# Kernel tuning notes

Measured on AMD Instinct MI355X. Metric: run time of the kernel, lower is better.

The kernel has to match this reference:

```python
import jax, jax.numpy as jnp
import numpy as np
import math

B, S, D, H = 4, 512, 1024, 16
DH = D // H
DQ = D // 4
MIN_STEPS, MAX_STEPS = 4, 12
THR = 1e-4


def lin(t, w, b):
    # torch Linear convention: w is (out, in)
    return jnp.einsum('...i,oi->...o', t, w) + b


def gelu(t):
    return jax.nn.gelu(t, approximate=False)  # torch nn.GELU() exact


def layernorm(t, g, b):
    m = t.mean(-1, keepdims=True)
    v = jnp.mean(jnp.square(t - m), axis=-1, keepdims=True)
    return (t - m) * jax.lax.rsqrt(v + 1e-5) * g + b


def _forward(h, x, ig_w1, ig_b1, ig_w2, ig_b2, wq, bq, wk, bk, wv, bv, wo, bo,
             g1_w1, g1_b1, g1_w2, g1_b2, gate_logits, ln_g, ln_b,
             sp_w1, sp_b1, sp_w2, sp_b2):
    # adaptive step count: steps = base + floor(sigmoid(MLP(mean_pool(h))).mean() * extra)
    pooled = h.mean(axis=1)  # (B, D)
    extra = jax.nn.sigmoid(lin(gelu(lin(pooled, sp_w1, sp_b1)), sp_w2, sp_b2)).mean()
    num_steps = jnp.minimum(
        MIN_STEPS + jnp.floor(extra * (MAX_STEPS - MIN_STEPS)).astype(jnp.int32), MAX_STEPS)

    gw = jax.nn.softmax(gate_logits)  # gate weights over the 3 gates
    scale = 1.0 / math.sqrt(DH)

    def step(carry, i):
        h, active = carry
        # G1 gate (G2/G3 multiply zero memory/expert outputs -> drop)
        G1 = jax.nn.sigmoid(lin(gelu(lin(h, g1_w1, g1_b1)), g1_w2, g1_b2)) * gw[0]
        # Phi: input-gated blend + raw multi-head self-attention
        gate = jax.nn.sigmoid(
            lin(gelu(lin(jnp.concatenate([h, x], axis=-1), ig_w1, ig_b1)), ig_w2, ig_b2))
        blended = gate * h + (1.0 - gate) * x
        q = lin(blended, wq, bq).reshape(B, S, H, DH)
        k = lin(blended, wk, bk).reshape(B, S, H, DH)
        v = lin(blended, wv, bv).reshape(B, S, H, DH)
        attn = jax.nn.softmax(jnp.einsum('bqhd,bkhd->bhqk', q, k) * scale, axis=-1)
        ctx = jnp.einsum('bhqk,bkhd->bqhd', attn, v).reshape(B, S, D)
        phi = lin(ctx, wo, bo)
        h_new = layernorm(h + G1 * phi, ln_g, ln_b)
        res = jnp.linalg.norm(h_new - h) / (jnp.linalg.norm(h) + 1e-8)
        act_i = active & (i < num_steps)
        h = jnp.where(act_i, h_new, h)
        active = act_i & jnp.logical_not((i >= MIN_STEPS) & (res < THR))
        return (h, active), None

    (h, _), _ = jax.lax.scan(step, (h, jnp.array(True)), jnp.arange(MAX_STEPS))
    return h


def setup_inputs() -> dict:
    key = jax.random.key(0)
    ks = jax.random.split(key, 16)
    f32 = jnp.float32

    def W(k, out_d, in_d):
        return jax.random.normal(k, (out_d, in_d), f32) * (1.0 / np.sqrt(in_d))

    return {
        'h': jax.random.normal(ks[0], (B, S, D), f32),
        'x': jax.random.normal(ks[1], (B, S, D), f32),
        # PhiLayer input_gate: Linear(2D, D/4) -> GELU -> Linear(D/4, D) -> Sigmoid
        'ig_w1': W(ks[2], DQ, 2 * D), 'ig_b1': jnp.zeros((DQ,), f32),
        'ig_w2': W(ks[3], D, DQ), 'ig_b2': jnp.zeros((D,), f32),
        # QKV / out projections (xavier-ish, zero bias)
        'wq': W(ks[4], D, D), 'bq': jnp.zeros((D,), f32),
        'wk': W(ks[5], D, D), 'bk': jnp.zeros((D,), f32),
        'wv': W(ks[6], D, D), 'bv': jnp.zeros((D,), f32),
        'wo': W(ks[7], D, D), 'bo': jnp.zeros((D,), f32),
        # Gating gate #1 MLP (only G1 contributes; memory/experts are zero)
        'g1_w1': W(ks[8], DQ, D), 'g1_b1': jnp.zeros((DQ,), f32),
        'g1_w2': W(ks[9], D, DQ), 'g1_b2': jnp.zeros((D,), f32),
        'gate_logits': jnp.ones((3,), f32),  # nn.Parameter(torch.ones(3))
        # LayerNorm
        'ln_g': jnp.ones((D,), f32), 'ln_b': jnp.zeros((D,), f32),
        # step predictor: Linear(D, D/4) -> GELU -> Linear(D/4, 1)
        'sp_w1': W(ks[10], DQ, D), 'sp_b1': jnp.zeros((DQ,), f32),
        'sp_w2': W(ks[11], 1, DQ), 'sp_b2': jnp.zeros((1,), f32),
    }


def reference(h, x, ig_w1, ig_b1, ig_w2, ig_b2, wq, bq, wk, bk, wv, bv, wo, bo,
              g1_w1, g1_b1, g1_w2, g1_b2, gate_logits, ln_g, ln_b,
              sp_w1, sp_b1, sp_w2, sp_b2):
    return _forward(h, x, ig_w1, ig_b1, ig_w2, ig_b2, wq, bq, wk, bk, wv, bv, wo, bo,
                    g1_w1, g1_b1, g1_w2, g1_b2, gate_logits, ln_g, ln_b,
                    sp_w1, sp_b1, sp_w2, sp_b2)
```

## Files before the change

kernel.cpp:

```cpp
#include <hip/hip_runtime.h>
#include <hip/hip_bf16.h>


#define B_   4
#define S_   512
#define D_   1024
#define H_   16
#define DH_  64
#define MSEQ 2048

typedef short short8 __attribute__((ext_vector_type(8)));
typedef float floatx4 __attribute__((ext_vector_type(4)));

static constexpr size_t OFF_H    = 0;
static constexpr size_t OFF_X    = 2097152;
static constexpr size_t OFF_HXB  = 4194304;
static constexpr size_t OFF_T2B  = 6291456;
static constexpr size_t OFF_T1B  = 6553600;
static constexpr size_t OFF_G1B  = 6815744;
static constexpr size_t OFF_QKVB = 7864320;
static constexpr size_t OFF_U    = 7864320;
static constexpr size_t OFF_CTXB = 11010048;
static constexpr size_t OFF_WARE = 12058624;
static constexpr size_t OFF_BIAS = 14811136;
static constexpr size_t OFF_POOL = 14817792;
static constexpr size_t OFF_SPT  = 14821888;
static constexpr size_t OFF_PPART= 14822912;
static constexpr size_t OFF_SCAL = 14888448;

static constexpr int W_WIG1 = 0;
static constexpr int W_WIG2 = 524288;
static constexpr int W_WG1  = 786432;
static constexpr int W_WG2  = 1048576;
static constexpr int W_QKV  = 1310720;
static constexpr int W_WO   = 4456448;
static constexpr int W_TOT  = 5505024;
static constexpr int B_TOT  = 6656;

__device__ __forceinline__ float bf2f(unsigned int u) {
  return __uint_as_float((u & 0xFFFFu) << 16);
}
__device__ __forceinline__ short f2bs(float f) {
  __hip_bfloat16 b = __float2bfloat16(f);
  return *reinterpret_cast<short*>(&b);
}
__device__ __forceinline__ unsigned int pk2(float lo, float hi) {
  return (unsigned int)(unsigned short)f2bs(lo) | ((unsigned int)(unsigned short)f2bs(hi) << 16);
}
__device__ __forceinline__ float ldf(const void* p, size_t i, int f32m) {
  return f32m ? ((const float*)p)[i] : bf2f(((const unsigned short*)p)[i]);
}
__device__ __forceinline__ float gelu_f(float x) {
  return 0.5f * x * (1.0f + erff(x * 0.70710678118654752440f));
}
__device__ __forceinline__ float sig_f(float x) {
  return 1.0f / (1.0f + expf(-x));
}
__device__ __forceinline__ void gl_lds16(const short* gp, short* lp) {
  __builtin_amdgcn_global_load_lds(
      (const __attribute__((address_space(1))) unsigned int*)gp,
      (__attribute__((address_space(3))) unsigned int*)lp, 16, 0, 0);
}
__device__ __forceinline__ float wave_sum(float v) {
  #pragma unroll
  for (int off = 32; off > 0; off >>= 1) v += __shfl_xor(v, off);
  return v;
}

__global__ void detect_kernel(const void* ln_g, int* dtf) {
  *dtf = (((const unsigned int*)ln_g)[0] == 0x3F800000u) ? 1 : 0;
}

struct RepackPtrs {
  const void* w[8];
  const void* b[8];
};

__global__ __launch_bounds__(256) void repack_all_kernel(
    const int* __restrict__ dtf, RepackPtrs ps,
    short* __restrict__ wdst, float* __restrict__ bdst) {
  const int f32m = *dtf;
  int i = blockIdx.x * 256 + threadIdx.x;
  if (i < W_TOT) {
    const int off[9] = {0, 524288, 786432, 1048576, 1310720, 2359296, 3407872, 4456448, W_TOT};
    int seg = 0;
    #pragma unroll
    for (int s = 1; s < 8; s++) seg += (i >= off[s]) ? 1 : 0;
    wdst[i] = f2bs(ldf(ps.w[seg], i - off[seg], f32m));
  } else if (i < W_TOT + B_TOT) {
    int j = i - W_TOT;
    const int off[9] = {0, 256, 1280, 1536, 2560, 3584, 4608, 5632, B_TOT};
    int seg = 0;
    #pragma unroll
    for (int s = 1; s < 8; s++) seg += (j >= off[s]) ? 1 : 0;
    bdst[j] = ldf(ps.b[seg], j - off[seg], f32m);
  }
}

__global__ __launch_bounds__(256) void cvt_in_kernel(
    const int* __restrict__ dtf, const void* __restrict__ hb,
    const void* __restrict__ xb, float* __restrict__ h, float* __restrict__ x,
    short* __restrict__ hxb, int n) {
  int f32m = *dtf;
  int i = blockIdx.x * 256 + threadIdx.x;
  if (i < n) {
    float hv = ldf(hb, i, f32m);
    float xv = ldf(xb, i, f32m);
    h[i] = hv;
    x[i] = xv;
    int row = i >> 10, col = i & 1023;
    hxb[(size_t)row * 2048 + col] = f2bs(hv);
    hxb[(size_t)row * 2048 + 1024 + col] = f2bs(xv);
  }
}

__global__ __launch_bounds__(256) void cvt_out_kernel(
    const int* __restrict__ dtf, const float* __restrict__ h, void* __restrict__ out, int n) {
  int f32m = *dtf;
  int i = blockIdx.x * 256 + threadIdx.x;
  if (i < n) {
    if (f32m) ((float*)out)[i] = h[i];
    else ((__hip_bfloat16*)out)[i] = __float2bfloat16(h[i]);
  }
}

__global__ __launch_bounds__(256) void pool_s1_kernel(
    const float* __restrict__ H, float* __restrict__ part) {
  int b = blockIdx.x, c = blockIdx.y, tid = threadIdx.x;
  const float* p = H + ((size_t)b * S_ + c * 32) * D_;
  #pragma unroll
  for (int rep = 0; rep < 4; rep++) {
    int d = rep * 256 + tid;
    float s = 0.f;
    for (int r = 0; r < 32; r++) s += p[(size_t)r * D_ + d];
    part[((size_t)b * 16 + c) * D_ + d] = s;
  }
}
__global__ __launch_bounds__(256) void pool_s2_kernel(
    const float* __restrict__ part, float* __restrict__ pooled) {
  int i = blockIdx.x * 256 + threadIdx.x;
  int b = i >> 10, d = i & 1023;
  float s = 0.f;
  #pragma unroll
  for (int c = 0; c < 16; c++) s += part[((size_t)b * 16 + c) * D_ + d];
  pooled[i] = s * (1.0f / (float)S_);
}

__device__ __forceinline__ float blk_sum256(float v, float* sm, int tid) {
  #pragma unroll
  for (int off = 32; off > 0; off >>= 1) v += __shfl_xor(v, off);
  __syncthreads();
  if ((tid & 63) == 0) sm[tid >> 6] = v;
  __syncthreads();
  return sm[0] + sm[1] + sm[2] + sm[3];
}

__global__ __launch_bounds__(256) void sp1_kernel(
    const int* __restrict__ dtf, const float* __restrict__ pooled,
    const void* __restrict__ w1, const void* __restrict__ b1,
    float* __restrict__ spt) {
  __shared__ float sm[4];
  const int f32m = *dtf;
  int j = blockIdx.x, tid = threadIdx.x;
  float s[4] = {0.f, 0.f, 0.f, 0.f};
  #pragma unroll
  for (int r = 0; r < 4; r++) {
    int k = tid * 4 + r;
    float w = ldf(w1, (size_t)j * D_ + k, f32m);
    s[0] += pooled[k] * w;
    s[1] += pooled[1024 + k] * w;
    s[2] += pooled[2048 + k] * w;
    s[3] += pooled[3072 + k] * w;
  }
  #pragma unroll
  for (int b = 0; b < 4; b++) {
    float t = blk_sum256(s[b], sm, tid);
    __syncthreads();
    if (tid == 0) spt[b * 256 + j] = gelu_f(t + ldf(b1, j, f32m));
  }
}

__global__ __launch_bounds__(256) void sp2_kernel(
    const int* __restrict__ dtf, const float* __restrict__ spt,
    const void* __restrict__ w2, const void* __restrict__ b2,
    const void* __restrict__ glog,
    int* __restrict__ num_steps, int* __restrict__ active,
    float* __restrict__ gw0, float* __restrict__ ssd, float* __restrict__ ssh) {
  __shared__ float z[4];
  const int f32m = *dtf;
  int tid = threadIdx.x;
  int wave = tid >> 6, lane = tid & 63;
  {
    int b = wave;
    float s = spt[b * 256 + lane]       * ldf(w2, lane, f32m) +
              spt[b * 256 + lane + 64]  * ldf(w2, lane + 64, f32m) +
              spt[b * 256 + lane + 128] * ldf(w2, lane + 128, f32m) +
              spt[b * 256 + lane + 192] * ldf(w2, lane + 192, f32m);
    #pragma unroll
    for (int off = 32; off > 0; off >>= 1) s += __shfl_xor(s, off);
    if (lane == 0) z[b] = sig_f(s + ldf(b2, 0, f32m));
  }
  __syncthreads();
  if (tid == 0) {
    float extra = 0.25f * (z[0] + z[1] + z[2] + z[3]);
    int ns = 4 + (int)floorf(extra * 8.0f);
    if (ns > 12) ns = 12;
    *num_steps = ns;
    *active = 1;
    *ssd = 0.f; *ssh = 0.f;
    float g0 = ldf(glog, 0, f32m);
    float g1 = ldf(glog, 1, f32m);
    float g2 = ldf(glog, 2, f32m);
    float mx = fmaxf(g0, fmaxf(g1, g2));
    float e0 = expf(g0 - mx), e1 = expf(g1 - mx), e2 = expf(g2 - mx);
    *gw0 = e0 / (e0 + e1 + e2);
  }
}

__global__ void control_kernel(int i, int* __restrict__ active, int* __restrict__ cur,
                               const int* __restrict__ num_steps,
                               float* __restrict__ ssd, float* __restrict__ ssh) {
  if (i > 0) {
    int prevf = *cur;
    if (prevf && (i - 1) >= 4) {
      float res = sqrtf(*ssd) / (sqrtf(*ssh) + 1e-8f);
      if (res < 1e-4f) *active = 0;
    }
  }
  *cur = ((*active) && (i < *num_steps)) ? 1 : 0;
  *ssd = 0.f; *ssh = 0.f;
}

enum { EPI_NONE = 0, EPI_GELU = 1, EPI_SIGSCALE = 2, EPI_BLEND = 3, EPI_RESADD = 4 };

template <int EPI, int BM, int BN>
__device__ __forceinline__ void mgemm_core(
    short* As, short* Bs,
    const short* __restrict__ A, int lda,
    const short* __restrict__ W, const float* __restrict__ bias, int K, int N,
    float* __restrict__ Cf, short* __restrict__ Cb,
    const float* __restrict__ aux1, const float* __restrict__ aux2f,
    const short* __restrict__ aux2b, const float* __restrict__ scale_ptr,
    int m0, int n0) {
  constexpr int FM = (BM / 2) / 16;
  constexpr int FN = (BN / 2) / 16;
  constexpr int CPA = (BM / 16) / 4;
  constexpr int CPB = (BN / 16) / 4;
  const int tid = threadIdx.x;
  const int lane = tid & 63, wv_ = tid >> 6;
  const int wm = (wv_ >> 1) * (BM / 2), wn = (wv_ & 1) * (BN / 2);
  const int srow = lane >> 2, scol = (lane & 3) * 8;
  const int frow = lane & 15, fk = (lane >> 4) * 8;

  floatx4 acc[FM][FN];
  #pragma unroll
  for (int i = 0; i < FM; i++)
    #pragma unroll
    for (int j = 0; j < FN; j++) acc[i][j] = (floatx4){0.f, 0.f, 0.f, 0.f};

  for (int k0 = 0; k0 < K; k0 += 32) {
    __syncthreads();
    #pragma unroll
    for (int c = 0; c < CPA; c++) {
      int q = wv_ * CPA + c;
      gl_lds16(A + (size_t)(m0 + q * 16 + srow) * lda + k0 + scol, As + q * 512);
    }
    #pragma unroll
    for (int c = 0; c < CPB; c++) {
      int q = wv_ * CPB + c;
      gl_lds16(W + (size_t)(n0 + q * 16 + srow) * K + k0 + scol, Bs + q * 512);
    }
    __syncthreads();
    short8 a[FM], b[FN];
    #pragma unroll
    for (int i = 0; i < FM; i++)
      a[i] = *reinterpret_cast<const short8*>(&As[(wm + i * 16 + frow) * 32 + fk]);
    #pragma unroll
    for (int j = 0; j < FN; j++)
      b[j] = *reinterpret_cast<const short8*>(&Bs[(wn + j * 16 + frow) * 32 + fk]);
    #pragma unroll
    for (int i = 0; i < FM; i++)
      #pragma unroll
      for (int j = 0; j < FN; j++)
        acc[i][j] = __builtin_amdgcn_mfma_f32_16x16x32_bf16(a[i], b[j], acc[i][j], 0, 0, 0);
  }

  float gwv = 0.f;
  if (EPI == EPI_SIGSCALE) gwv = *scale_ptr;
  const int rq = (lane >> 4) * 4;
  #pragma unroll
  for (int i = 0; i < FM; i++) {
    #pragma unroll
    for (int j = 0; j < FN; j++) {
      int n = n0 + wn + j * 16 + (lane & 15);
      float bv = bias[n];
      #pragma unroll
      for (int r = 0; r < 4; r++) {
        int m = m0 + wm + i * 16 + rq + r;
        size_t off = (size_t)m * N + n;
        float v = acc[i][j][r] + bv;
        if (EPI == EPI_GELU) {
          Cb[off] = f2bs(gelu_f(v));
        } else if (EPI == EPI_SIGSCALE) {
          Cb[off] = f2bs(sig_f(v) * gwv);
        } else if (EPI == EPI_BLEND) {
          float s = sig_f(v);
          Cb[off] = f2bs(s * aux1[off] + (1.f - s) * aux2f[off]);
        } else if (EPI == EPI_RESADD) {
          Cf[off] = aux1[off] + bf2f((unsigned short)aux2b[off]) * v;
        } else {
          Cb[off] = f2bs(v);
        }
      }
    }
  }
}

template <int EPI, int BM, int BN>
__global__ __launch_bounds__(256) void mgemm(
    const int* __restrict__ flag, const short* __restrict__ A, int lda,
    const short* __restrict__ W, const float* __restrict__ bias, int K, int N,
    float* __restrict__ Cf, short* __restrict__ Cb,
    const float* __restrict__ aux1, const float* __restrict__ aux2f,
    const short* __restrict__ aux2b, const float* __restrict__ scale_ptr) {
  if (*flag == 0) return;
  __shared__ short As[BM * 32];
  __shared__ short Bs[BN * 32];
  mgemm_core<EPI, BM, BN>(As, Bs, A, lda, W, bias, K, N, Cf, Cb,
                          aux1, aux2f, aux2b, scale_ptr,
                          blockIdx.y * BM, blockIdx.x * BN);
}

__global__ __launch_bounds__(256) void gate1_kernel(
    const int* __restrict__ flag, const short* __restrict__ hxb,
    const short* __restrict__ warena, const float* __restrict__ biasA,
    short* __restrict__ t2b, short* __restrict__ t1b) {
  if (*flag == 0) return;
  __shared__ short As[64 * 32];
  __shared__ short Bs[64 * 32];
  if (blockIdx.z == 0)
    mgemm_core<EPI_GELU, 64, 64>(As, Bs, hxb, 2048, warena + W_WIG1, biasA + 0,
                                 2048, 256, nullptr, t2b, nullptr, nullptr, nullptr,
                                 nullptr, blockIdx.y * 64, blockIdx.x * 64);
  else
    mgemm_core<EPI_GELU, 64, 64>(As, Bs, hxb, 2048, warena + W_WG1, biasA + 1280,
                                 1024, 256, nullptr, t1b, nullptr, nullptr, nullptr,
                                 nullptr, blockIdx.y * 64, blockIdx.x * 64);
}

__global__ __launch_bounds__(256) void gate2_kernel(
    const int* __restrict__ flag, const short* __restrict__ t2b,
    const short* __restrict__ t1b, const short* __restrict__ warena,
    const float* __restrict__ biasA, short* __restrict__ bldb,
    short* __restrict__ g1b, const float* __restrict__ h,
    const float* __restrict__ xf, const float* __restrict__ gw0) {
  if (*flag == 0) return;
  __shared__ short As[128 * 32];
  __shared__ short Bs[64 * 32];
  if (blockIdx.z == 0)
    mgemm_core<EPI_BLEND, 128, 64>(As, Bs, t2b, 256, warena + W_WIG2, biasA + 256,
                                   256, 1024, nullptr, bldb, h, xf, nullptr,
                                   nullptr, blockIdx.y * 128, blockIdx.x * 64);
  else
    mgemm_core<EPI_SIGSCALE, 128, 64>(As, Bs, t1b, 256, warena + W_WG2, biasA + 1536,
                                      256, 1024, nullptr, g1b, nullptr, nullptr,
                                      nullptr, gw0, blockIdx.y * 128, blockIdx.x * 64);
}

#define AP_ 72
__global__ __launch_bounds__(256) void attn_kernel(
    const int* __restrict__ flag, const short* __restrict__ qkv,
    short* __restrict__ ctxb) {
  if (*flag == 0) return;
  __shared__ short Ks[64 * AP_];
  __shared__ short Vt[64 * AP_];
  __shared__ short Ps[64 * AP_];
  const int tid = threadIdx.x;
  const int lane = tid & 63, wv = tid >> 6;
  const int ln15 = lane & 15, quad = lane >> 4;
  const int qt = blockIdx.x, hh = blockIdx.y, b = blockIdx.z;
  const int wm = wv * 16;
  const size_t rowbase = (size_t)b * S_;
  const int hcol = hh * DH_;
  const float scale = 0.125f;

  short8 qa[2];
  {
    const short* qp = qkv + (rowbase + qt * 64 + wm + ln15) * 3072 + hcol + quad * 8;
    qa[0] = *reinterpret_cast<const short8*>(qp);
    qa[1] = *reinterpret_cast<const short8*>(qp + 32);
  }
  const int skk = tid >> 2, scg = (tid & 3) * 16;

  float mrow[4] = {-1e30f, -1e30f, -1e30f, -1e30f};
  float lrow[4] = {0.f, 0.f, 0.f, 0.f};
  floatx4 accO[4];
  #pragma unroll
  for (int j = 0; j < 4; j++) accO[j] = (floatx4){0.f, 0.f, 0.f, 0.f};

  for (int kt = 0; kt < 8; kt++) {
    __syncthreads();
    {
      const short* gk = qkv + (rowbase + kt * 64 + skk) * 3072 + 1024 + hcol + scg;
      uint4 k0 = *reinterpret_cast<const uint4*>(gk);
      uint4 k1 = *reinterpret_cast<const uint4*>(gk + 8);
      *reinterpret_cast<uint4*>(&Ks[skk * AP_ + scg]) = k0;
      *reinterpret_cast<uint4*>(&Ks[skk * AP_ + scg + 8]) = k1;
      short8 v0 = *reinterpret_cast<const short8*>(gk + 1024);
      short8 v1 = *reinterpret_cast<const short8*>(gk + 1032);
      #pragma unroll
      for (int j = 0; j < 8; j++) Vt[(scg + j) * AP_ + skk] = v0[j];
      #pragma unroll
      for (int j = 0; j < 8; j++) Vt[(scg + 8 + j) * AP_ + skk] = v1[j];
    }
    __syncthreads();

    floatx4 sc[4];
    #pragma unroll
    for (int nf = 0; nf < 4; nf++) {
      short8 b0 = *reinterpret_cast<const short8*>(&Ks[(nf * 16 + ln15) * AP_ + quad * 8]);
      short8 b1 = *reinterpret_cast<const short8*>(&Ks[(nf * 16 + ln15) * AP_ + 32 + quad * 8]);
      floatx4 s = (floatx4){0.f, 0.f, 0.f, 0.f};
      s = __builtin_amdgcn_mfma_f32_16x16x32_bf16(qa[0], b0, s, 0, 0, 0);
      s = __builtin_amdgcn_mfma_f32_16x16x32_bf16(qa[1], b1, s, 0, 0, 0);
      sc[nf] = s;
    }

    float prob[4][4];
    #pragma unroll
    for (int r = 0; r < 4; r++) {
      float lm = fmaxf(fmaxf(sc[0][r], sc[1][r]), fmaxf(sc[2][r], sc[3][r])) * scale;
      lm = fmaxf(lm, __shfl_xor(lm, 1));
      lm = fmaxf(lm, __shfl_xor(lm, 2));
      lm = fmaxf(lm, __shfl_xor(lm, 4));
      lm = fmaxf(lm, __shfl_xor(lm, 8));
      float mn = fmaxf(mrow[r], lm);
      float alpha = expf(mrow[r] - mn);
      float ls = 0.f;
      #pragma unroll
      for (int nf = 0; nf < 4; nf++) {
        float p = expf(sc[nf][r] * scale - mn);
        prob[nf][r] = p;
        ls += p;
      }
      ls += __shfl_xor(ls, 1);
      ls += __shfl_xor(ls, 2);
      ls += __shfl_xor(ls, 4);
      ls += __shfl_xor(ls, 8);
      lrow[r] = lrow[r] * alpha + ls;
      mrow[r] = mn;
      #pragma unroll
      for (int df = 0; df < 4; df++) accO[df][r] *= alpha;
    }
    #pragma unroll
    for (int nf = 0; nf < 4; nf++)
      #pragma unroll
      for (int r = 0; r < 4; r++)
        Ps[(wm + quad * 4 + r) * AP_ + nf * 16 + ln15] = f2bs(prob[nf][r]);
    __syncthreads();

    short8 pa0 = *reinterpret_cast<const short8*>(&Ps[(wm + ln15) * AP_ + quad * 8]);
    short8 pa1 = *reinterpret_cast<const short8*>(&Ps[(wm + ln15) * AP_ + 32 + quad * 8]);
    #pragma unroll
    for (int df = 0; df < 4; df++) {
      short8 bv0 = *reinterpret_cast<const short8*>(&Vt[(df * 16 + ln15) * AP_ + quad * 8]);
      short8 bv1 = *reinterpret_cast<const short8*>(&Vt[(df * 16 + ln15) * AP_ + 32 + quad * 8]);
      accO[df] = __builtin_amdgcn_mfma_f32_16x16x32_bf16(pa0, bv0, accO[df], 0, 0, 0);
      accO[df] = __builtin_amdgcn_mfma_f32_16x16x32_bf16(pa1, bv1, accO[df], 0, 0, 0);
    }
  }

  float inv[4];
  #pragma unroll
  for (int r = 0; r < 4; r++) inv[r] = 1.0f / lrow[r];
  #pragma unroll
  for (int df = 0; df < 4; df++) {
    #pragma unroll
    for (int r = 0; r < 4; r++) {
      size_t off = (rowbase + qt * 64 + wm + quad * 4 + r) * 1024 + hcol + df * 16 + ln15;
      ctxb[off] = f2bs(accO[df][r] * inv[r]);
    }
  }
}

__global__ __launch_bounds__(256) void ln_kernel(
    const int* __restrict__ flag, const int* __restrict__ dtf,
    const float* __restrict__ U, float* __restrict__ H, short* __restrict__ hxb,
    const void* __restrict__ g, const void* __restrict__ be,
    float* __restrict__ ssd, float* __restrict__ ssh) {
  if (*flag == 0) return;
  const int f32m = *dtf;
  __shared__ float sdd[4], sdh[4];
  const int tid = threadIdx.x;
  const int wv = tid >> 6, lane = tid & 63;
  const int row = blockIdx.x * 4 + wv;
  const float4* u4 = reinterpret_cast<const float4*>(U + (size_t)row * D_);
  float4* h4 = reinterpret_cast<float4*>(H + (size_t)row * D_);
  float4 uv[4], hv[4];
  #pragma unroll
  for (int j = 0; j < 4; j++) uv[j] = u4[lane + 64 * j];
  #pragma unroll
  for (int j = 0; j < 4; j++) hv[j] = h4[lane + 64 * j];
  float s = 0.f;
  #pragma unroll
  for (int j = 0; j < 4; j++) s += (uv[j].x + uv[j].y) + (uv[j].z + uv[j].w);
  s = wave_sum(s);
  float mean = s * (1.0f / (float)D_);
  float4 d[4];
  float vv = 0.f;
  #pragma unroll
  for (int j = 0; j < 4; j++) {
    d[j].x = uv[j].x - mean; d[j].y = uv[j].y - mean;
    d[j].z = uv[j].z - mean; d[j].w = uv[j].w - mean;
    vv += d[j].x * d[j].x + d[j].y * d[j].y + d[j].z * d[j].z + d[j].w * d[j].w;
  }
  vv = wave_sum(vv);
  float rstd = rsqrtf(vv * (1.0f / (float)D_) + 1e-5f);
  float lsd = 0.f, lsh = 0.f;
  #pragma unroll
  for (int j = 0; j < 4; j++) {
    int c = (lane + 64 * j) * 4;
    float hn0 = d[j].x * rstd * ldf(g, c + 0, f32m) + ldf(be, c + 0, f32m);
    float hn1 = d[j].y * rstd * ldf(g, c + 1, f32m) + ldf(be, c + 1, f32m);
    float hn2 = d[j].z * rstd * ldf(g, c + 2, f32m) + ldf(be, c + 2, f32m);
    float hn3 = d[j].w * rstd * ldf(g, c + 3, f32m) + ldf(be, c + 3, f32m);
    float e0 = hn0 - hv[j].x, e1 = hn1 - hv[j].y, e2 = hn2 - hv[j].z, e3 = hn3 - hv[j].w;
    lsd += e0 * e0 + e1 * e1 + e2 * e2 + e3 * e3;
    lsh += hv[j].x * hv[j].x + hv[j].y * hv[j].y + hv[j].z * hv[j].z + hv[j].w * hv[j].w;
    h4[lane + 64 * j] = make_float4(hn0, hn1, hn2, hn3);
    uint2 pw;
    pw.x = pk2(hn0, hn1);
    pw.y = pk2(hn2, hn3);
    *reinterpret_cast<uint2*>(hxb + (size_t)row * 2048 + c) = pw;
  }
  lsd = wave_sum(lsd);
  lsh = wave_sum(lsh);
  if (lane == 0) { sdd[wv] = lsd; sdh[wv] = lsh; }
  __syncthreads();
  if (tid == 0) {
    atomicAdd(ssd, (sdd[0] + sdd[1]) + (sdd[2] + sdd[3]));
    atomicAdd(ssh, (sdh[0] + sdh[1]) + (sdh[2] + sdh[3]));
  }
}

extern "C" void kernel_launch(void* const* d_in, const int* in_sizes, int n_in,
                              void* d_out, int out_size, void* d_ws, size_t ws_size,
                              hipStream_t stream) {
  (void)in_sizes; (void)n_in; (void)out_size; (void)ws_size;
  const void* h_in  = d_in[0];
  const void* x_in  = d_in[1];
  const void* glog  = d_in[18];
  const void* ln_g  = d_in[19];
  const void* ln_b  = d_in[20];
  const void* sp_w1 = d_in[21];
  const void* sp_b1 = d_in[22];
  const void* sp_w2 = d_in[23];
  const void* sp_b2 = d_in[24];

  RepackPtrs rp;
  rp.w[0] = d_in[2];  rp.w[1] = d_in[4];  rp.w[2] = d_in[14]; rp.w[3] = d_in[16];
  rp.w[4] = d_in[6];  rp.w[5] = d_in[8];  rp.w[6] = d_in[10]; rp.w[7] = d_in[12];
  rp.b[0] = d_in[3];  rp.b[1] = d_in[5];  rp.b[2] = d_in[15]; rp.b[3] = d_in[17];
  rp.b[4] = d_in[7];  rp.b[5] = d_in[9];  rp.b[6] = d_in[11]; rp.b[7] = d_in[13];

  float* wsf = (float*)d_ws;
  float* h      = wsf + OFF_H;
  float* xf     = wsf + OFF_X;
  short* hxb    = (short*)(wsf + OFF_HXB);
  short* t2b    = (short*)(wsf + OFF_T2B);
  short* t1b    = (short*)(wsf + OFF_T1B);
  short* g1b    = (short*)(wsf + OFF_G1B);
  short* qkvb   = (short*)(wsf + OFF_QKVB);
  float* u      = wsf + OFF_U;
  short* ctxb   = (short*)(wsf + OFF_CTXB);
  short* bldb   = ctxb;
  short* warena = (short*)(wsf + OFF_WARE);
  float* biasA  = wsf + OFF_BIAS;
  float* pooled = wsf + OFF_POOL;
  float* spt    = wsf + OFF_SPT;
  float* ppart  = wsf + OFF_PPART;
  float* ssd    = wsf + OFF_SCAL + 0;
  float* ssh    = wsf + OFF_SCAL + 1;
  float* gw0    = wsf + OFF_SCAL + 2;
  int* ip        = (int*)(wsf + OFF_SCAL + 8);
  int* num_steps = ip + 0;
  int* active    = ip + 1;
  int* cur       = ip + 2;
  int* dtf       = ip + 3;

  const int NTOT = B_ * S_ * D_;

  detect_kernel<<<1, 1, 0, stream>>>(ln_g, dtf);
  repack_all_kernel<<<(W_TOT + B_TOT + 255) / 256, 256, 0, stream>>>(dtf, rp, warena, biasA);
  cvt_in_kernel<<<NTOT / 256, 256, 0, stream>>>(dtf, h_in, x_in, h, xf, hxb, NTOT);
  pool_s1_kernel<<<dim3(4, 16), 256, 0, stream>>>(h, ppart);
  pool_s2_kernel<<<16, 256, 0, stream>>>(ppart, pooled);
  sp1_kernel<<<256, 256, 0, stream>>>(dtf, pooled, sp_w1, sp_b1, spt);
  sp2_kernel<<<1, 256, 0, stream>>>(dtf, spt, sp_w2, sp_b2, glog,
                                    num_steps, active, gw0, ssd, ssh);
  for (int i = 0; i < 12; i++) {
    control_kernel<<<1, 1, 0, stream>>>(i, active, cur, num_steps, ssd, ssh);
    gate1_kernel<<<dim3(4, 32, 2), 256, 0, stream>>>(cur, hxb, warena, biasA, t2b, t1b);
    gate2_kernel<<<dim3(16, 16, 2), 256, 0, stream>>>(cur, t2b, t1b, warena, biasA,
                                                      bldb, g1b, h, xf, gw0);
    mgemm<EPI_NONE, 128, 64><<<dim3(48, 16), 256, 0, stream>>>(
        cur, bldb, 1024, warena + W_QKV, biasA + 2560, 1024, 3072,
        nullptr, qkvb, nullptr, nullptr, nullptr, nullptr);
    attn_kernel<<<dim3(8, 16, 4), 256, 0, stream>>>(cur, qkvb, ctxb);
    mgemm<EPI_RESADD, 128, 64><<<dim3(16, 16), 256, 0, stream>>>(
        cur, ctxb, 1024, warena + W_WO, biasA + 5632, 1024, 1024,
        u, nullptr, h, nullptr, g1b, nullptr);
    ln_kernel<<<512, 256, 0, stream>>>(cur, dtf, u, h, hxb, ln_g, ln_b, ssd, ssh);
  }
  cvt_out_kernel<<<NTOT / 256, 256, 0, stream>>>(dtf, h, (void*)d_out, NTOT);
}
```

Before: 1.334 ms.

## Double GEMM K-tile to 64 and fold step control into layernorm kernel

The bf16 MFMA GEMM core now stages 64 columns of K per iteration as two 32-wide halves in shared memory. This halves the number of barrier-separated load/compute rounds and doubles the LDS footprint per block. The separate single-thread control kernel launched every step is removed. Its convergence check and the update of the next step's active flag now run in the last-finishing block of the layernorm kernel, found with a per-step atomic counter. This saves one launch per iteration and relies on a threadfence plus atomic ordering across blocks.

```diff
diff --git a/kernel.cpp b/kernel.cpp
--- a/kernel.cpp
+++ b/kernel.cpp
@@ -184,11 +184,13 @@
     const int* __restrict__ dtf, const float* __restrict__ spt,
     const void* __restrict__ w2, const void* __restrict__ b2,
     const void* __restrict__ glog,
-    int* __restrict__ num_steps, int* __restrict__ active,
-    float* __restrict__ gw0, float* __restrict__ ssd, float* __restrict__ ssh) {
+    int* __restrict__ num_steps, int* __restrict__ active, int* __restrict__ cur,
+    float* __restrict__ gw0, float* __restrict__ ssd, float* __restrict__ ssh,
+    int* __restrict__ cnt) {
   __shared__ float z[4];
   const int f32m = *dtf;
   int tid = threadIdx.x;
+  if (tid < 12) cnt[tid] = 0;
   int wave = tid >> 6, lane = tid & 63;
   {
     int b = wave;
@@ -207,6 +209,7 @@
     if (ns > 12) ns = 12;
     *num_steps = ns;
     *active = 1;
+    *cur = 1;
     *ssd = 0.f; *ssh = 0.f;
     float g0 = ldf(glog, 0, f32m);
     float g1 = ldf(glog, 1, f32m);
@@ -215,20 +218,6 @@
     float e0 = expf(g0 - mx), e1 = expf(g1 - mx), e2 = expf(g2 - mx);
     *gw0 = e0 / (e0 + e1 + e2);
   }
-}
-
-__global__ void control_kernel(int i, int* __restrict__ active, int* __restrict__ cur,
-                               const int* __restrict__ num_steps,
-                               float* __restrict__ ssd, float* __restrict__ ssh) {
-  if (i > 0) {
-    int prevf = *cur;
-    if (prevf && (i - 1) >= 4) {
-      float res = sqrtf(*ssd) / (sqrtf(*ssh) + 1e-8f);
-      if (res < 1e-4f) *active = 0;
-    }
-  }
-  *cur = ((*active) && (i < *num_steps)) ? 1 : 0;
-  *ssd = 0.f; *ssh = 0.f;
 }
 
 enum { EPI_NONE = 0, EPI_GELU = 1, EPI_SIGSCALE = 2, EPI_BLEND = 3, EPI_RESADD = 4 };
@@ -258,31 +247,40 @@
     #pragma unroll
     for (int j = 0; j < FN; j++) acc[i][j] = (floatx4){0.f, 0.f, 0.f, 0.f};
 
-  for (int k0 = 0; k0 < K; k0 += 32) {
+  for (int k0 = 0; k0 < K; k0 += 64) {
     __syncthreads();
     #pragma unroll
     for (int c = 0; c < CPA; c++) {
       int q = wv_ * CPA + c;
-      gl_lds16(A + (size_t)(m0 + q * 16 + srow) * lda + k0 + scol, As + q * 512);
+      const short* gp = A + (size_t)(m0 + q * 16 + srow) * lda + k0 + scol;
+      gl_lds16(gp, As + q * 512);
+      gl_lds16(gp + 32, As + BM * 32 + q * 512);
     }
     #pragma unroll
     for (int c = 0; c < CPB; c++) {
       int q = wv_ * CPB + c;
-      gl_lds16(W + (size_t)(n0 + q * 16 + srow) * K + k0 + scol, Bs + q * 512);
+      const short* gp = W + (size_t)(n0 + q * 16 + srow) * K + k0 + scol;
+      gl_lds16(gp, Bs + q * 512);
+      gl_lds16(gp + 32, Bs + BN * 32 + q * 512);
     }
     __syncthreads();
-    short8 a[FM], b[FN];
-    #pragma unroll
-    for (int i = 0; i < FM; i++)
-      a[i] = *reinterpret_cast<const short8*>(&As[(wm + i * 16 + frow) * 32 + fk]);
-    #pragma unroll
-    for (int j = 0; j < FN; j++)
-      b[j] = *reinterpret_cast<const short8*>(&Bs[(wn + j * 16 + frow) * 32 + fk]);
-    #pragma unroll
-    for (int i = 0; i < FM; i++)
+    #pragma unroll
+    for (int hlf = 0; hlf < 2; hlf++) {
+      const short* Ah = As + hlf * BM * 32;
+      const short* Bh = Bs + hlf * BN * 32;
+      short8 a[FM], b[FN];
+      #pragma unroll
+      for (int i = 0; i < FM; i++)
+        a[i] = *reinterpret_cast<const short8*>(&Ah[(wm + i * 16 + frow) * 32 + fk]);
       #pragma unroll
       for (int j = 0; j < FN; j++)
-        acc[i][j] = __builtin_amdgcn_mfma_f32_16x16x32_bf16(a[i], b[j], acc[i][j], 0, 0, 0);
+        b[j] = *reinterpret_cast<const short8*>(&Bh[(wn + j * 16 + frow) * 32 + fk]);
+      #pragma unroll
+      for (int i = 0; i < FM; i++)
+        #pragma unroll
+        for (int j = 0; j < FN; j++)
+          acc[i][j] = __builtin_amdgcn_mfma_f32_16x16x32_bf16(a[i], b[j], acc[i][j], 0, 0, 0);
+    }
   }
 
   float gwv = 0.f;
@@ -324,8 +322,8 @@
     const float* __restrict__ aux1, const float* __restrict__ aux2f,
     const short* __restrict__ aux2b, const float* __restrict__ scale_ptr) {
   if (*flag == 0) return;
-  __shared__ short As[BM * 32];
-  __shared__ short Bs[BN * 32];
+  __shared__ short As[BM * 64];
+  __shared__ short Bs[BN * 64];
   mgemm_core<EPI, BM, BN>(As, Bs, A, lda, W, bias, K, N, Cf, Cb,
                           aux1, aux2f, aux2b, scale_ptr,
                           blockIdx.y * BM, blockIdx.x * BN);
@@ -336,8 +334,8 @@
     const short* __restrict__ warena, const float* __restrict__ biasA,
     short* __restrict__ t2b, short* __restrict__ t1b) {
   if (*flag == 0) return;
-  __shared__ short As[64 * 32];
-  __shared__ short Bs[64 * 32];
+  __shared__ short As[64 * 64];
+  __shared__ short Bs[64 * 64];
   if (blockIdx.z == 0)
     mgemm_core<EPI_GELU, 64, 64>(As, Bs, hxb, 2048, warena + W_WIG1, biasA + 0,
                                  2048, 256, nullptr, t2b, nullptr, nullptr, nullptr,
@@ -355,8 +353,8 @@
     short* __restrict__ g1b, const float* __restrict__ h,
     const float* __restrict__ xf, const float* __restrict__ gw0) {
   if (*flag == 0) return;
-  __shared__ short As[128 * 32];
-  __shared__ short Bs[64 * 32];
+  __shared__ short As[128 * 64];
+  __shared__ short Bs[64 * 64];
   if (blockIdx.z == 0)
     mgemm_core<EPI_BLEND, 128, 64>(As, Bs, t2b, 256, warena + W_WIG2, biasA + 256,
                                    256, 1024, nullptr, bldb, h, xf, nullptr,
@@ -484,62 +482,80 @@
 }
 
 __global__ __launch_bounds__(256) void ln_kernel(
-    const int* __restrict__ flag, const int* __restrict__ dtf,
+    int step_i, const int* __restrict__ flagp, const int* __restrict__ dtf,
     const float* __restrict__ U, float* __restrict__ H, short* __restrict__ hxb,
     const void* __restrict__ g, const void* __restrict__ be,
-    float* __restrict__ ssd, float* __restrict__ ssh) {
-  if (*flag == 0) return;
+    float* __restrict__ ssd, float* __restrict__ ssh,
+    int* __restrict__ active, int* __restrict__ cur,
+    const int* __restrict__ num_steps, int* __restrict__ cnt) {
+  const int flag = *flagp;
   const int f32m = *dtf;
   __shared__ float sdd[4], sdh[4];
   const int tid = threadIdx.x;
   const int wv = tid >> 6, lane = tid & 63;
-  const int row = blockIdx.x * 4 + wv;
-  const float4* u4 = reinterpret_cast<const float4*>(U + (size_t)row * D_);
-  float4* h4 = reinterpret_cast<float4*>(H + (size_t)row * D_);
-  float4 uv[4], hv[4];
-  #pragma unroll
-  for (int j = 0; j < 4; j++) uv[j] = u4[lane + 64 * j];
-  #pragma unroll
-  for (int j = 0; j < 4; j++) hv[j] = h4[lane + 64 * j];
-  float s = 0.f;
-  #pragma unroll
-  for (int j = 0; j < 4; j++) s += (uv[j].x + uv[j].y) + (uv[j].z + uv[j].w);
-  s = wave_sum(s);
-  float mean = s * (1.0f / (float)D_);
-  float4 d[4];
-  float vv = 0.f;
-  #pragma unroll
-  for (int j = 0; j < 4; j++) {
-    d[j].x = uv[j].x - mean; d[j].y = uv[j].y - mean;
-    d[j].z = uv[j].z - mean; d[j].w = uv[j].w - mean;
-    vv += d[j].x * d[j].x + d[j].y * d[j].y + d[j].z * d[j].z + d[j].w * d[j].w;
-  }
-  vv = wave_sum(vv);
-  float rstd = rsqrtf(vv * (1.0f / (float)D_) + 1e-5f);
-  float lsd = 0.f, lsh = 0.f;
-  #pragma unroll
-  for (int j = 0; j < 4; j++) {
-    int c = (lane + 64 * j) * 4;
-    float hn0 = d[j].x * rstd * ldf(g, c + 0, f32m) + ldf(be, c + 0, f32m);
-    float hn1 = d[j].y * rstd * ldf(g, c + 1, f32m) + ldf(be, c + 1, f32m);
-    float hn2 = d[j].z * rstd * ldf(g, c + 2, f32m) + ldf(be, c + 2, f32m);
-    float hn3 = d[j].w * rstd * ldf(g, c + 3, f32m) + ldf(be, c + 3, f32m);
-    float e0 = hn0 - hv[j].x, e1 = hn1 - hv[j].y, e2 = hn2 - hv[j].z, e3 = hn3 - hv[j].w;
-    lsd += e0 * e0 + e1 * e1 + e2 * e2 + e3 * e3;
-    lsh += hv[j].x * hv[j].x + hv[j].y * hv[j].y + hv[j].z * hv[j].z + hv[j].w * hv[j].w;
-    h4[lane + 64 * j] = make_float4(hn0, hn1, hn2, hn3);
-    uint2 pw;
-    pw.x = pk2(hn0, hn1);
-    pw.y = pk2(hn2, hn3);
-    *reinterpret_cast<uint2*>(hxb + (size_t)row * 2048 + c) = pw;
-  }
-  lsd = wave_sum(lsd);
-  lsh = wave_sum(lsh);
-  if (lane == 0) { sdd[wv] = lsd; sdh[wv] = lsh; }
-  __syncthreads();
+  if (flag) {
+    const int row = blockIdx.x * 4 + wv;
+    const float4* u4 = reinterpret_cast<const float4*>(U + (size_t)row * D_);
+    float4* h4 = reinterpret_cast<float4*>(H + (size_t)row * D_);
+    float4 uv[4], hv[4];
+    #pragma unroll
+    for (int j = 0; j < 4; j++) uv[j] = u4[lane + 64 * j];
+    #pragma unroll
+    for (int j = 0; j < 4; j++) hv[j] = h4[lane + 64 * j];
+    float s = 0.f;
+    #pragma unroll
+    for (int j = 0; j < 4; j++) s += (uv[j].x + uv[j].y) + (uv[j].z + uv[j].w);
+    s = wave_sum(s);
+    float mean = s * (1.0f / (float)D_);
+    float4 d[4];
+    float vv = 0.f;
+    #pragma unroll
+    for (int j = 0; j < 4; j++) {
+      d[j].x = uv[j].x - mean; d[j].y = uv[j].y - mean;
+      d[j].z = uv[j].z - mean; d[j].w = uv[j].w - mean;
+      vv += d[j].x * d[j].x + d[j].y * d[j].y + d[j].z * d[j].z + d[j].w * d[j].w;
+    }
+    vv = wave_sum(vv);
+    float rstd = rsqrtf(vv * (1.0f / (float)D_) + 1e-5f);
+    float lsd = 0.f, lsh = 0.f;
+    #pragma unroll
+    for (int j = 0; j < 4; j++) {
+      int c = (lane + 64 * j) * 4;
+      float hn0 = d[j].x * rstd * ldf(g, c + 0, f32m) + ldf(be, c + 0, f32m);
+      float hn1 = d[j].y * rstd * ldf(g, c + 1, f32m) + ldf(be, c + 1, f32m);
+      float hn2 = d[j].z * rstd * ldf(g, c + 2, f32m) + ldf(be, c + 2, f32m);
+      float hn3 = d[j].w * rstd * ldf(g, c + 3, f32m) + ldf(be, c + 3, f32m);
+      float e0 = hn0 - hv[j].x, e1 = hn1 - hv[j].y, e2 = hn2 - hv[j].z, e3 = hn3 - hv[j].w;
+      lsd += e0 * e0 + e1 * e1 + e2 * e2 + e3 * e3;
+      lsh += hv[j].x * hv[j].x + hv[j].y * hv[j].y + hv[j].z * hv[j].z + hv[j].w * hv[j].w;
+      h4[lane + 64 * j] = make_float4(hn0, hn1, hn2, hn3);
+      uint2 pw;
+      pw.x = pk2(hn0, hn1);
+      pw.y = pk2(hn2, hn3);
+      *reinterpret_cast<uint2*>(hxb + (size_t)row * 2048 + c) = pw;
+    }
+    lsd = wave_sum(lsd);
+    lsh = wave_sum(lsh);
+    if (lane == 0) { sdd[wv] = lsd; sdh[wv] = lsh; }
+    __syncthreads();
+    if (tid == 0) {
+      atomicAdd(ssd, (sdd[0] + sdd[1]) + (sdd[2] + sdd[3]));
+      atomicAdd(ssh, (sdh[0] + sdh[1]) + (sdh[2] + sdh[3]));
+    }
+  }
   if (tid == 0) {
-    atomicAdd(ssd, (sdd[0] + sdd[1]) + (sdd[2] + sdd[3]));
-    atomicAdd(ssh, (sdh[0] + sdh[1]) + (sdh[2] + sdh[3]));
+    __threadfence();
+    int old = atomicAdd(&cnt[step_i], 1);
+    if (old == (int)gridDim.x - 1) {
+      if (flag && step_i >= 4) {
+        float nd = atomicAdd(ssd, 0.0f);
+        float nh = atomicAdd(ssh, 0.0f);
+        float res = sqrtf(nd) / (sqrtf(nh) + 1e-8f);
+        if (res < 1e-4f) *active = 0;
+      }
+      *cur = ((*active) && (step_i + 1 < *num_steps)) ? 1 : 0;
+      *ssd = 0.f; *ssh = 0.f;
+    }
   }
 }
 
@@ -587,6 +603,7 @@
   int* active    = ip + 1;
   int* cur       = ip + 2;
   int* dtf       = ip + 3;
+  int* cnt       = ip + 4;
 
   const int NTOT = B_ * S_ * D_;
 
@@ -597,9 +614,8 @@
   pool_s2_kernel<<<16, 256, 0, stream>>>(ppart, pooled);
   sp1_kernel<<<256, 256, 0, stream>>>(dtf, pooled, sp_w1, sp_b1, spt);
   sp2_kernel<<<1, 256, 0, stream>>>(dtf, spt, sp_w2, sp_b2, glog,
-                                    num_steps, active, gw0, ssd, ssh);
+                                    num_steps, active, cur, gw0, ssd, ssh, cnt);
   for (int i = 0; i < 12; i++) {
-    control_kernel<<<1, 1, 0, stream>>>(i, active, cur, num_steps, ssd, ssh);
     gate1_kernel<<<dim3(4, 32, 2), 256, 0, stream>>>(cur, hxb, warena, biasA, t2b, t1b);
     gate2_kernel<<<dim3(16, 16, 2), 256, 0, stream>>>(cur, t2b, t1b, warena, biasA,
                                                       bldb, g1b, h, xf, gw0);
@@ -610,7 +626,8 @@
     mgemm<EPI_RESADD, 128, 64><<<dim3(16, 16), 256, 0, stream>>>(
         cur, ctxb, 1024, warena + W_WO, biasA + 5632, 1024, 1024,
         u, nullptr, h, nullptr, g1b, nullptr);
-    ln_kernel<<<512, 256, 0, stream>>>(cur, dtf, u, h, hxb, ln_g, ln_b, ssd, ssh);
+    ln_kernel<<<512, 256, 0, stream>>>(i, cur, dtf, u, h, hxb, ln_g, ln_b,
+                                       ssd, ssh, active, cur, num_steps, cnt);
   }
   cvt_out_kernel<<<NTOT / 256, 256, 0, stream>>>(dtf, h, (void*)d_out, NTOT);
 }
```

Result: faster. 1.275 ms (-4.4%).
